# Kernel tuning notes

Measured on AMD Instinct MI355X. Metric: run time of the kernel, lower is better.

## Reference

```python
import jax, jax.numpy as jnp
import numpy as np

N_NODES = 100000
N_EDGES = 1600000
D_IN = 64
D_HID = 64
EPS = 0.0  # dgl GINConv default: init_eps=0, learn_eps=False


def setup_inputs() -> dict:
    key = jax.random.key(0)
    k1, k2, k3, k4, k5 = jax.random.split(key, 5)
    x = jax.random.normal(k1, (N_NODES, D_IN), dtype=jnp.float32)
    src = jax.random.randint(k2, (N_EDGES,), 0, N_NODES, dtype=jnp.int32)
    dst = jax.random.randint(k3, (N_EDGES,), 0, N_NODES, dtype=jnp.int32)
    # nn.Linear-style init scale
    W1 = jax.random.normal(k4, (D_IN, D_HID), dtype=jnp.float32) / np.sqrt(D_IN)
    b1 = jnp.zeros((D_HID,), dtype=jnp.float32)
    W2 = jax.random.normal(k5, (D_HID, D_HID), dtype=jnp.float32) / np.sqrt(D_HID)
    b2 = jnp.zeros((D_HID,), dtype=jnp.float32)
    return {"x": x, "src": src, "dst": dst, "W1": W1, "b1": b1, "W2": W2, "b2": b2}


def _gin_layer(h, src, dst, W, b):
    # sum-aggregate messages from src -> dst (graph SpMM), then (1+eps)*h + agg,
    # then dense linear + ReLU — matches dgl GINConv(aggregator_type='sum', activation=ReLU)
    agg = jax.ops.segment_sum(h[src], dst, num_segments=N_NODES)  # [N, D]
    return jax.nn.relu(((1.0 + EPS) * h + agg) @ W + b)


def reference(x, src, dst, W1, b1, W2, b2):
    h = _gin_layer(x, src, dst, W1, b1)
    h = _gin_layer(h, src, dst, W2, b2)
    return h
```

## Files before the change

### kernel.cpp

```cpp
#include <hip/hip_runtime.h>
#include <hip/hip_bf16.h>


#define D 64
#define ROWS_PER_BLOCK 32
#define CHSZ 4096
#define NPBS 512
#define SBSHIFT 9
#define MAXNBS 256
#define MAXNCH 512

typedef unsigned short ushort_t;

__device__ inline unsigned short f2bf(float f) {
    unsigned u = __float_as_uint(f);
    return (unsigned short)((u + 0x7fff + ((u >> 16) & 1)) >> 16);
}

__device__ inline void acc8(float* acc, uint4 v) {
    acc[0] += __uint_as_float(v.x << 16);
    acc[1] += __uint_as_float(v.x & 0xffff0000u);
    acc[2] += __uint_as_float(v.y << 16);
    acc[3] += __uint_as_float(v.y & 0xffff0000u);
    acc[4] += __uint_as_float(v.z << 16);
    acc[5] += __uint_as_float(v.z & 0xffff0000u);
    acc[6] += __uint_as_float(v.w << 16);
    acc[7] += __uint_as_float(v.w & 0xffff0000u);
}

__device__ inline void unpack8(float* v, uint4 u) {
    v[0] = __uint_as_float(u.x << 16); v[1] = __uint_as_float(u.x & 0xffff0000u);
    v[2] = __uint_as_float(u.y << 16); v[3] = __uint_as_float(u.y & 0xffff0000u);
    v[4] = __uint_as_float(u.z << 16); v[5] = __uint_as_float(u.z & 0xffff0000u);
    v[6] = __uint_as_float(u.w << 16); v[7] = __uint_as_float(u.w & 0xffff0000u);
}


__global__ __launch_bounds__(256) void to_bf16z(const float4* __restrict__ in,
                                                uint2* __restrict__ out, int n4,
                                                int* __restrict__ total, int nbs) {
    int i = blockIdx.x * 256 + threadIdx.x;
    if (blockIdx.x == 0)
        for (int j = threadIdx.x; j < nbs; j += 256) total[j] = 0;
    if (i >= n4) return;
    float4 v = in[i];
    out[i] = make_uint2((unsigned)f2bf(v.x) | ((unsigned)f2bf(v.y) << 16),
                        (unsigned)f2bf(v.z) | ((unsigned)f2bf(v.w) << 16));
}

__global__ __launch_bounds__(512) void k1_hist(const int* __restrict__ dst,
                                               int* __restrict__ hist,
                                               int* __restrict__ total,
                                               int n_edges, int nch, int nbs) {
    __shared__ int lh[MAXNBS];
    for (int i = threadIdx.x; i < nbs; i += 512) lh[i] = 0;
    __syncthreads();
    int base = blockIdx.x * CHSZ;
    int lim = min(CHSZ, n_edges - base);
    for (int k = threadIdx.x; k < lim; k += 512)
        atomicAdd(&lh[dst[base + k] >> SBSHIFT], 1);
    __syncthreads();
    for (int i = threadIdx.x; i < nbs; i += 512) {
        int v = lh[i];
        hist[i * nch + blockIdx.x] = v;
        if (v) atomicAdd(&total[i], v);
    }
}

__global__ __launch_bounds__(256) void k2c_rowscan(int* __restrict__ hist,
                                                   const int* __restrict__ total,
                                                   int* __restrict__ sstart,
                                                   int nch, int nbs, int n_edges) {
    __shared__ int tt[256];
    __shared__ int t[MAXNCH];
    int b = blockIdx.x;
    int tid = threadIdx.x;

    tt[tid] = (tid < nbs) ? total[tid] : 0;
    __syncthreads();
    for (int off = 1; off < 256; off <<= 1) {
        int v = (tid >= off) ? tt[tid - off] : 0;
        __syncthreads();
        tt[tid] += v;
        __syncthreads();
    }
    int base = (b == 0) ? 0 : tt[b - 1];
    if (tid == 0) {
        sstart[b] = base;
        if (b == 0) sstart[nbs] = n_edges;
    }

    int* row = hist + (size_t)b * nch;
    int nround = (nch + 255) & ~255;
    for (int i = tid; i < nround; i += 256) t[i] = (i < nch) ? row[i] : 0;
    __syncthreads();
    for (int off = 1; off < nround; off <<= 1) {
        int v[MAXNCH / 256];
        for (int i = tid, j = 0; i < nround; i += 256, ++j)
            v[j] = (i >= off) ? t[i - off] : 0;
        __syncthreads();
        for (int i = tid, j = 0; i < nround; i += 256, ++j) t[i] += v[j];
        __syncthreads();
    }
    for (int i = tid; i < nch; i += 256)
        row[i] = base + ((i == 0) ? 0 : t[i - 1]);
}

__global__ __launch_bounds__(512) void k3_scatter(const int* __restrict__ src,
                                                  const int* __restrict__ dst,
                                                  const int* __restrict__ hist,
                                                  unsigned* __restrict__ tmp,
                                                  int n_edges, int nch, int nbs) {
    __shared__ int lcur[MAXNBS];
    int c = blockIdx.x;
    for (int i = threadIdx.x; i < nbs; i += 512) lcur[i] = hist[i * nch + c];
    __syncthreads();
    int base = c * CHSZ;
    int lim = min(CHSZ, n_edges - base);
    for (int k = threadIdx.x; k < lim; k += 512) {
        int d = dst[base + k];
        int s = src[base + k];
        int pos = atomicAdd(&lcur[d >> SBSHIFT], 1);
        tmp[pos] = ((unsigned)(d & (NPBS - 1)) << 18) | (unsigned)s;
    }
}

__global__ __launch_bounds__(512) void k4_fine(const unsigned* __restrict__ tmp,
                                               const int* __restrict__ sstart,
                                               int* __restrict__ esrc,
                                               int* __restrict__ offs,
                                               int n_nodes) {
    __shared__ int lcnt[NPBS];
    __shared__ int lcur[NPBS];
    __shared__ int tsum[256];

    int b = blockIdx.x;
    int tid = threadIdx.x;
    int base = sstart[b];
    int cnt = sstart[b + 1] - base;

    lcnt[tid] = 0;
    __syncthreads();

    for (int i = tid; i < cnt; i += 512)
        atomicAdd(&lcnt[tmp[base + i] >> 18], 1);
    __syncthreads();

    int a0 = 0, a1 = 0;
    if (tid < 256) {
        a0 = lcnt[2 * tid];
        a1 = lcnt[2 * tid + 1];
        tsum[tid] = a0 + a1;
    }
    __syncthreads();
    for (int off = 1; off < 256; off <<= 1) {
        int v = 0;
        if (tid < 256 && tid >= off) v = tsum[tid - off];
        __syncthreads();
        if (tid < 256) tsum[tid] += v;
        __syncthreads();
    }
    if (tid < 256) {
        int ex = (tid == 0) ? 0 : tsum[tid - 1];
        lcur[2 * tid] = ex;
        lcur[2 * tid + 1] = ex + a0;
        int node = b * NPBS + 2 * tid;
        if (node <= n_nodes) offs[node] = base + ex;
        if (node + 1 <= n_nodes) offs[node + 1] = base + ex + a0;
    }
    __syncthreads();

    for (int i = tid; i < cnt; i += 512) {
        unsigned p = tmp[base + i];
        int pos = atomicAdd(&lcur[p >> 18], 1);
        esrc[base + pos] = (int)((p & 0x3FFFFu) << 3);
    }
}


__global__ __launch_bounds__(128) void gin_agg_bf(const uint4* __restrict__ hb,
                                                  const int* __restrict__ offs,
                                                  const int* __restrict__ esrc,
                                                  uint4* __restrict__ aggb,
                                                  int n_nodes) {
    int t = blockIdx.x * 128 + threadIdx.x;
    int n = t >> 2;
    if (n >= n_nodes) return;
    int c2 = (t & 3) * 2;
    const uint4* selfp = hb + (size_t)n * 8 + c2;
    float acc[16];
#pragma unroll
    for (int j = 0; j < 16; ++j) acc[j] = 0.0f;
    {
        uint4 s0 = selfp[0], s1 = selfp[1];
        acc8(acc, s0); acc8(acc + 8, s1);
    }

    int i = offs[n];
    int end = offs[n + 1];

    for (; i + 8 <= end; i += 8) {
        uint4 v[16];
#pragma unroll
        for (int j = 0; j < 8; ++j) {
            const uint4* r = hb + (size_t)(unsigned)esrc[i + j] + c2;
            v[2 * j]     = r[0];
            v[2 * j + 1] = r[1];
        }
#pragma unroll
        for (int j = 0; j < 8; ++j) {
            acc8(acc, v[2 * j]);
            acc8(acc + 8, v[2 * j + 1]);
        }
    }
    if (i + 4 <= end) {
        uint4 v[8];
#pragma unroll
        for (int j = 0; j < 4; ++j) {
            const uint4* r = hb + (size_t)(unsigned)esrc[i + j] + c2;
            v[2 * j]     = r[0];
            v[2 * j + 1] = r[1];
        }
#pragma unroll
        for (int j = 0; j < 4; ++j) {
            acc8(acc, v[2 * j]);
            acc8(acc + 8, v[2 * j + 1]);
        }
        i += 4;
    }
    for (; i < end; ++i) {
        const uint4* r = hb + (size_t)(unsigned)esrc[i] + c2;
        uint4 a = r[0], b = r[1];
        acc8(acc, a); acc8(acc + 8, b);
    }

    uint4 o0, o1;
    o0.x = (unsigned)f2bf(acc[0])  | ((unsigned)f2bf(acc[1])  << 16);
    o0.y = (unsigned)f2bf(acc[2])  | ((unsigned)f2bf(acc[3])  << 16);
    o0.z = (unsigned)f2bf(acc[4])  | ((unsigned)f2bf(acc[5])  << 16);
    o0.w = (unsigned)f2bf(acc[6])  | ((unsigned)f2bf(acc[7])  << 16);
    o1.x = (unsigned)f2bf(acc[8])  | ((unsigned)f2bf(acc[9])  << 16);
    o1.y = (unsigned)f2bf(acc[10]) | ((unsigned)f2bf(acc[11]) << 16);
    o1.z = (unsigned)f2bf(acc[12]) | ((unsigned)f2bf(acc[13]) << 16);
    o1.w = (unsigned)f2bf(acc[14]) | ((unsigned)f2bf(acc[15]) << 16);
    aggb[(size_t)n * 8 + c2]     = o0;
    aggb[(size_t)n * 8 + c2 + 1] = o1;
}

#define RSTRIDE (D + 4)
template <bool BF16OUT>
__global__ __launch_bounds__(256) void gin_mlp(const uint4* __restrict__ hs,
                                               const float* __restrict__ W,
                                               const float* __restrict__ b,
                                               void* __restrict__ out_,
                                               int n_nodes) {
    __shared__ float Wl[D * D];
    __shared__ float bl[D];
    __shared__ float rows[ROWS_PER_BLOCK * RSTRIDE];

    int tid = threadIdx.x;

    const float4* W4 = (const float4*)W;
    float4* Wl4 = (float4*)Wl;
#pragma unroll
    for (int i = 0; i < 4; ++i) Wl4[tid + 256 * i] = W4[tid + 256 * i];
    if (tid < D / 4) ((float4*)bl)[tid] = ((const float4*)b)[tid];

    size_t row0 = (size_t)blockIdx.x * ROWS_PER_BLOCK;
    {
        uint4 u = hs[row0 * 8 + tid];
        float v[8];
        unpack8(v, u);
        int r = tid >> 3;
        int col = (tid & 7) * 8;
        float* dstp = rows + r * RSTRIDE + col;
#pragma unroll
        for (int j = 0; j < 8; ++j) dstp[j] = v[j];
    }
    __syncthreads();

    int lane = tid & 63;
    int w = tid >> 6;

    float acc[8];
#pragma unroll
    for (int r = 0; r < 8; ++r) acc[r] = bl[lane];

#pragma unroll
    for (int k = 0; k < D; ++k) {
        float wv = Wl[k * D + lane];
#pragma unroll
        for (int r = 0; r < 8; ++r)
            acc[r] = fmaf(rows[(w * 8 + r) * RSTRIDE + k], wv, acc[r]);
    }

#pragma unroll
    for (int r = 0; r < 8; ++r) {
        float v = acc[r] > 0.0f ? acc[r] : 0.0f;
        size_t idx = (row0 + (size_t)w * 8 + r) * D + lane;
        if (BF16OUT) ((ushort_t*)out_)[idx] = f2bf(v);
        else         ((float*)out_)[idx] = v;
    }
}

extern "C" void kernel_launch(void* const* d_in, const int* in_sizes, int n_in,
                              void* d_out, int out_size, void* d_ws, size_t ws_size,
                              hipStream_t stream) {
    const float* x   = (const float*)d_in[0];
    const int*   src = (const int*)d_in[1];
    const int*   dst = (const int*)d_in[2];
    const float* W1  = (const float*)d_in[3];
    const float* b1  = (const float*)d_in[4];
    const float* W2  = (const float*)d_in[5];
    const float* b2  = (const float*)d_in[6];
    float* out = (float*)d_out;

    const int n_nodes = in_sizes[0] / D;
    const int n_edges = in_sizes[1];
    const int nch = (n_edges + CHSZ - 1) / CHSZ;
    const int nbs = (n_nodes + NPBS - 1) / NPBS;

    ushort_t* Ab     = (ushort_t*)d_ws;
    ushort_t* hb     = Ab + (size_t)n_nodes * D;
    int*      offs   = (int*)(hb + (size_t)n_nodes * D);
    int*      sstart = offs + (n_nodes + 1);
    int*      total  = sstart + (nbs + 1);
    int*      hist   = total + nbs;
    unsigned* tmp    = (unsigned*)(hist + (size_t)nbs * nch);
    int*      esrc   = (int*)(tmp + n_edges);

    const int agg_blocks = (n_nodes * 4 + 127) / 128;
    const int mlp_blocks = (n_nodes + ROWS_PER_BLOCK - 1) / ROWS_PER_BLOCK;
    const int cvt_blocks = (n_nodes * (D / 4) + 255) / 256;

    to_bf16z<<<cvt_blocks, 256, 0, stream>>>((const float4*)x, (uint2*)hb,
                                             n_nodes * (D / 4), total, nbs);
    k1_hist<<<nch, 512, 0, stream>>>(dst, hist, total, n_edges, nch, nbs);
    k2c_rowscan<<<nbs, 256, 0, stream>>>(hist, total, sstart, nch, nbs, n_edges);
    k3_scatter<<<nch, 512, 0, stream>>>(src, dst, hist, tmp, n_edges, nch, nbs);
    k4_fine<<<nbs, 512, 0, stream>>>(tmp, sstart, esrc, offs, n_nodes);

    gin_agg_bf<<<agg_blocks, 128, 0, stream>>>((const uint4*)hb, offs, esrc,
                                               (uint4*)Ab, n_nodes);
    gin_mlp<true><<<mlp_blocks, 256, 0, stream>>>((const uint4*)Ab, W1, b1,
                                                  hb, n_nodes);

    gin_agg_bf<<<agg_blocks, 128, 0, stream>>>((const uint4*)hb, offs, esrc,
                                               (uint4*)Ab, n_nodes);
    gin_mlp<false><<<mlp_blocks, 256, 0, stream>>>((const uint4*)Ab, W2, b2,
                                                   out, n_nodes);
}
```

Baseline: 186.7 us.

## Split bf16 node features into four column slabs for cache-local aggregation

Node features are stored as four column slabs of 16 bf16 values each, and the aggregation kernel runs one pass per slab. Block order puts all blocks of one slab before the next, so each pass gathers from a 3.2MB working set that can stay in L2 instead of the full 12.8MB array. The conversion, MLP input load and layer-1 output store are rewritten for the slab layout. The cost is reading CSR offsets and edge indices four times and issuing more, smaller 32-byte gathers per edge.

```diff
diff --git a/kernel.cpp b/kernel.cpp
--- a/kernel.cpp
+++ b/kernel.cpp
@@ -9,6 +9,7 @@
 #define SBSHIFT 9
 #define MAXNBS 256
 #define MAXNCH 512
+#define NSLAB 4
 
 typedef unsigned short ushort_t;
 
@@ -37,15 +38,21 @@
 
 
 __global__ __launch_bounds__(256) void to_bf16z(const float4* __restrict__ in,
-                                                uint2* __restrict__ out, int n4,
-                                                int* __restrict__ total, int nbs) {
+                                                uint2* __restrict__ outs, int n4,
+                                                int* __restrict__ total, int nbs,
+                                                int n_nodes) {
     int i = blockIdx.x * 256 + threadIdx.x;
     if (blockIdx.x == 0)
         for (int j = threadIdx.x; j < nbs; j += 256) total[j] = 0;
     if (i >= n4) return;
     float4 v = in[i];
-    out[i] = make_uint2((unsigned)f2bf(v.x) | ((unsigned)f2bf(v.y) << 16),
-                        (unsigned)f2bf(v.z) | ((unsigned)f2bf(v.w) << 16));
+    int n = i >> 4;
+    int q = i & 15;
+    int p = q >> 2;
+    int u2i = q & 3;
+    outs[(size_t)p * n_nodes * 4 + n * 4 + u2i] =
+        make_uint2((unsigned)f2bf(v.x) | ((unsigned)f2bf(v.y) << 16),
+                   (unsigned)f2bf(v.z) | ((unsigned)f2bf(v.w) << 16));
 }
 
 __global__ __launch_bounds__(512) void k1_hist(const int* __restrict__ dst,
@@ -173,83 +180,62 @@
     for (int i = tid; i < cnt; i += 512) {
         unsigned p = tmp[base + i];
         int pos = atomicAdd(&lcur[p >> 18], 1);
-        esrc[base + pos] = (int)((p & 0x3FFFFu) << 3);
-    }
-}
-
-
-__global__ __launch_bounds__(128) void gin_agg_bf(const uint4* __restrict__ hb,
-                                                  const int* __restrict__ offs,
-                                                  const int* __restrict__ esrc,
-                                                  uint4* __restrict__ aggb,
-                                                  int n_nodes) {
-    int t = blockIdx.x * 128 + threadIdx.x;
-    int n = t >> 2;
+        esrc[base + pos] = (int)((p & 0x3FFFFu) << 1);
+    }
+}
+
+
+__global__ __launch_bounds__(256) void gin_agg_slab(const uint4* __restrict__ hbs,
+                                                    const int* __restrict__ offs,
+                                                    const int* __restrict__ esrc,
+                                                    uint4* __restrict__ abs_,
+                                                    int n_nodes, int nblk) {
+    int pass = blockIdx.x / nblk;
+    int t = (blockIdx.x - pass * nblk) * 256 + threadIdx.x;
+    int n = t >> 1;
     if (n >= n_nodes) return;
-    int c2 = (t & 3) * 2;
-    const uint4* selfp = hb + (size_t)n * 8 + c2;
-    float acc[16];
-#pragma unroll
-    for (int j = 0; j < 16; ++j) acc[j] = 0.0f;
-    {
-        uint4 s0 = selfp[0], s1 = selfp[1];
-        acc8(acc, s0); acc8(acc + 8, s1);
-    }
+    int c = t & 1;
+    const uint4* slab = hbs + (size_t)pass * n_nodes * 2;
+
+    float acc[8];
+#pragma unroll
+    for (int j = 0; j < 8; ++j) acc[j] = 0.0f;
+    acc8(acc, slab[n * 2 + c]);
 
     int i = offs[n];
     int end = offs[n + 1];
 
     for (; i + 8 <= end; i += 8) {
-        uint4 v[16];
-#pragma unroll
-        for (int j = 0; j < 8; ++j) {
-            const uint4* r = hb + (size_t)(unsigned)esrc[i + j] + c2;
-            v[2 * j]     = r[0];
-            v[2 * j + 1] = r[1];
-        }
-#pragma unroll
-        for (int j = 0; j < 8; ++j) {
-            acc8(acc, v[2 * j]);
-            acc8(acc + 8, v[2 * j + 1]);
-        }
+        uint4 v[8];
+#pragma unroll
+        for (int j = 0; j < 8; ++j)
+            v[j] = slab[(unsigned)esrc[i + j] + c];
+#pragma unroll
+        for (int j = 0; j < 8; ++j) acc8(acc, v[j]);
     }
     if (i + 4 <= end) {
-        uint4 v[8];
-#pragma unroll
-        for (int j = 0; j < 4; ++j) {
-            const uint4* r = hb + (size_t)(unsigned)esrc[i + j] + c2;
-            v[2 * j]     = r[0];
-            v[2 * j + 1] = r[1];
-        }
-#pragma unroll
-        for (int j = 0; j < 4; ++j) {
-            acc8(acc, v[2 * j]);
-            acc8(acc + 8, v[2 * j + 1]);
-        }
+        uint4 v[4];
+#pragma unroll
+        for (int j = 0; j < 4; ++j)
+            v[j] = slab[(unsigned)esrc[i + j] + c];
+#pragma unroll
+        for (int j = 0; j < 4; ++j) acc8(acc, v[j]);
         i += 4;
     }
-    for (; i < end; ++i) {
-        const uint4* r = hb + (size_t)(unsigned)esrc[i] + c2;
-        uint4 a = r[0], b = r[1];
-        acc8(acc, a); acc8(acc + 8, b);
-    }
-
-    uint4 o0, o1;
-    o0.x = (unsigned)f2bf(acc[0])  | ((unsigned)f2bf(acc[1])  << 16);
-    o0.y = (unsigned)f2bf(acc[2])  | ((unsigned)f2bf(acc[3])  << 16);
-    o0.z = (unsigned)f2bf(acc[4])  | ((unsigned)f2bf(acc[5])  << 16);
-    o0.w = (unsigned)f2bf(acc[6])  | ((unsigned)f2bf(acc[7])  << 16);
-    o1.x = (unsigned)f2bf(acc[8])  | ((unsigned)f2bf(acc[9])  << 16);
-    o1.y = (unsigned)f2bf(acc[10]) | ((unsigned)f2bf(acc[11]) << 16);
-    o1.z = (unsigned)f2bf(acc[12]) | ((unsigned)f2bf(acc[13]) << 16);
-    o1.w = (unsigned)f2bf(acc[14]) | ((unsigned)f2bf(acc[15]) << 16);
-    aggb[(size_t)n * 8 + c2]     = o0;
-    aggb[(size_t)n * 8 + c2 + 1] = o1;
+    for (; i < end; ++i)
+        acc8(acc, slab[(unsigned)esrc[i] + c]);
+
+    uint4 o;
+    o.x = (unsigned)f2bf(acc[0]) | ((unsigned)f2bf(acc[1]) << 16);
+    o.y = (unsigned)f2bf(acc[2]) | ((unsigned)f2bf(acc[3]) << 16);
+    o.z = (unsigned)f2bf(acc[4]) | ((unsigned)f2bf(acc[5]) << 16);
+    o.w = (unsigned)f2bf(acc[6]) | ((unsigned)f2bf(acc[7]) << 16);
+    abs_[(size_t)pass * n_nodes * 2 + n * 2 + c] = o;
 }
 
 #define RSTRIDE (D + 4)
 template <bool BF16OUT>
-__global__ __launch_bounds__(256) void gin_mlp(const uint4* __restrict__ hs,
+__global__ __launch_bounds__(256) void gin_mlp(const uint4* __restrict__ hss,
                                                const float* __restrict__ W,
                                                const float* __restrict__ b,
                                                void* __restrict__ out_,
@@ -268,12 +254,13 @@
 
     size_t row0 = (size_t)blockIdx.x * ROWS_PER_BLOCK;
     {
-        uint4 u = hs[row0 * 8 + tid];
+        int r = tid >> 3;
+        int p = (tid >> 1) & 3;
+        int half = tid & 1;
+        uint4 u = hss[(size_t)p * n_nodes * 2 + (row0 + r) * 2 + half];
         float v[8];
         unpack8(v, u);
-        int r = tid >> 3;
-        int col = (tid & 7) * 8;
-        float* dstp = rows + r * RSTRIDE + col;
+        float* dstp = rows + r * RSTRIDE + p * 16 + half * 8;
 #pragma unroll
         for (int j = 0; j < 8; ++j) dstp[j] = v[j];
     }
@@ -297,9 +284,14 @@
 #pragma unroll
     for (int r = 0; r < 8; ++r) {
         float v = acc[r] > 0.0f ? acc[r] : 0.0f;
-        size_t idx = (row0 + (size_t)w * 8 + r) * D + lane;
-        if (BF16OUT) ((ushort_t*)out_)[idx] = f2bf(v);
-        else         ((float*)out_)[idx] = v;
+        size_t node = row0 + (size_t)w * 8 + r;
+        if (BF16OUT) {
+            int p = lane >> 4;
+            int cin = lane & 15;
+            ((ushort_t*)out_)[(size_t)p * n_nodes * 16 + node * 16 + cin] = f2bf(v);
+        } else {
+            ((float*)out_)[node * D + lane] = v;
+        }
     }
 }
 
@@ -329,24 +321,27 @@
     unsigned* tmp    = (unsigned*)(hist + (size_t)nbs * nch);
     int*      esrc   = (int*)(tmp + n_edges);
 
-    const int agg_blocks = (n_nodes * 4 + 127) / 128;
+    const int agg_nblk = (n_nodes * 2 + 255) / 256;
     const int mlp_blocks = (n_nodes + ROWS_PER_BLOCK - 1) / ROWS_PER_BLOCK;
     const int cvt_blocks = (n_nodes * (D / 4) + 255) / 256;
 
     to_bf16z<<<cvt_blocks, 256, 0, stream>>>((const float4*)x, (uint2*)hb,
-                                             n_nodes * (D / 4), total, nbs);
+                                             n_nodes * (D / 4), total, nbs,
+                                             n_nodes);
     k1_hist<<<nch, 512, 0, stream>>>(dst, hist, total, n_edges, nch, nbs);
     k2c_rowscan<<<nbs, 256, 0, stream>>>(hist, total, sstart, nch, nbs, n_edges);
     k3_scatter<<<nch, 512, 0, stream>>>(src, dst, hist, tmp, n_edges, nch, nbs);
     k4_fine<<<nbs, 512, 0, stream>>>(tmp, sstart, esrc, offs, n_nodes);
 
-    gin_agg_bf<<<agg_blocks, 128, 0, stream>>>((const uint4*)hb, offs, esrc,
-                                               (uint4*)Ab, n_nodes);
+    gin_agg_slab<<<agg_nblk * NSLAB, 256, 0, stream>>>((const uint4*)hb, offs,
+                                                       esrc, (uint4*)Ab,
+                                                       n_nodes, agg_nblk);
     gin_mlp<true><<<mlp_blocks, 256, 0, stream>>>((const uint4*)Ab, W1, b1,
                                                   hb, n_nodes);
 
-    gin_agg_bf<<<agg_blocks, 128, 0, stream>>>((const uint4*)hb, offs, esrc,
-                                               (uint4*)Ab, n_nodes);
+    gin_agg_slab<<<agg_nblk * NSLAB, 256, 0, stream>>>((const uint4*)hb, offs,
+                                                       esrc, (uint4*)Ab,
+                                                       n_nodes, agg_nblk);
     gin_mlp<false><<<mlp_blocks, 256, 0, stream>>>((const uint4*)Ab, W2, b2,
                                                    out, n_nodes);
 }
```

Result: slower. 242.6 us (+30.0%).
